# Performance work log

Measured on AMD Instinct MI355X. Metric: run time of the kernel, lower is better.

The kernel has to match this reference:

```python
import jax, jax.numpy as jnp
import numpy as np

B, T, D, R = 8, 2048, 2048, 4


def setup_inputs() -> dict:
    key = jax.random.key(0)
    ks = jax.random.split(key, 9)
    u = jax.random.normal(ks[0], (B, T, D), dtype=jnp.float32)
    # a chosen so tanh(a) ~ 0.995: keeps cumprod over T=2048 away from underflow
    a = 3.0 + 0.2 * jax.random.uniform(ks[1], (D,), dtype=jnp.float32)
    b = 0.02 * jax.random.normal(ks[2], (D,), dtype=jnp.float32)
    c = 0.02 * jax.random.normal(ks[3], (D,), dtype=jnp.float32)
    d = 0.02 * jax.random.normal(ks[4], (D,), dtype=jnp.float32)
    gate_w = jax.random.normal(ks[5], (D, D), dtype=jnp.float32) / np.float32(np.sqrt(D))
    gate_b = jnp.zeros((D,), dtype=jnp.float32)
    d_lr_u = 0.02 * jax.random.normal(ks[6], (D, R), dtype=jnp.float32)
    d_lr_v = 0.02 * jax.random.normal(ks[7], (R, D), dtype=jnp.float32)
    return {"u": u, "a": a, "b": b, "c": c, "d": d,
            "gate_w": gate_w, "gate_b": gate_b,
            "d_lr_u": d_lr_u, "d_lr_v": d_lr_v}


def reference(u, a, b, c, d, gate_w, gate_b, d_lr_u, d_lr_v):
    # u: [B,T,D]
    Bs, Ts, Ds = u.shape
    rank = d_lr_u.shape[1]
    # gated input (torch Linear: x @ W.T + bias)
    g = jax.nn.sigmoid(jnp.einsum('btd,ed->bte', u, gate_w) + gate_b)
    u_g = u * g
    aa = jnp.tanh(a)                                   # [D], in (-1,1)
    # low-rank correction to feedthrough d
    u_mean = jnp.mean(u_g, axis=1, keepdims=True)      # [B,1,D]
    d_lr = (u_mean @ d_lr_u) @ d_lr_v / max(1.0, float(rank))
    d_eff = d + d_lr                                   # [B,1,D]
    # diagonal SSM via cumprod/cumsum (G[t] = aa^(t+1)); per-channel, T-independent of B
    G = jnp.cumprod(jnp.broadcast_to(aa, (Ts, Ds)), axis=0)  # [T,D]
    bu = b * u_g                                       # [B,T,D]
    G_safe = G.at[0].set(jnp.maximum(G[0], 1e-6))
    z = bu / G_safe                                    # [B,T,D]
    s = G * jnp.cumsum(z, axis=1)                      # [B,T,D]
    y = c * s + d_eff * u_g
    return y
```

## Files before the change

kernel.cpp:

```cpp
#include <hip/hip_runtime.h>
#include <hip/hip_bf16.h>
#include <math.h>

#define Bq 8
#define Tq 2048
#define Dq 2048
#define Rq 4
#define Mq (Bq*Tq)
#define NC 16
#define CL (Tq/NC)

typedef __attribute__((ext_vector_type(8))) short bf16x8;
typedef __attribute__((ext_vector_type(4))) float f32x4;
typedef __attribute__((ext_vector_type(4))) unsigned short us4;

__device__ __forceinline__ unsigned short f2bf(float x) {
    unsigned int u = __float_as_uint(x);
    unsigned int r = (u + 0x7fffu + ((u >> 16) & 1u)) >> 16;
    return (unsigned short)r;
}
__device__ __forceinline__ float bf2f(unsigned short h) {
    return __uint_as_float((unsigned)h << 16);
}

template<int UGBF>
__device__ __forceinline__ f32x4 ld4(const void* p, long long off) {
    if constexpr (UGBF) {
        us4 v = *(const us4*)((const unsigned short*)p + off);
        f32x4 r;
        r.x = bf2f(v.x); r.y = bf2f(v.y); r.z = bf2f(v.z); r.w = bf2f(v.w);
        return r;
    } else {
        return *(const f32x4*)((const float*)p + off);
    }
}

__global__ __launch_bounds__(256) void k0_convert(
    const float* __restrict__ u, const float* __restrict__ gw,
    const float* __restrict__ a,
    unsigned short* __restrict__ ubf, unsigned short* __restrict__ wbf,
    float* __restrict__ aat, float* __restrict__ aaLt)
{
    const long long uN4 = (long long)Mq * Dq / 4;
    const long long wN4 = (long long)Dq * Dq / 4;
    long long gid = (long long)blockIdx.x * blockDim.x + threadIdx.x;
    if (gid < Dq) {
        float aa = tanhf(a[gid]);
        aat[gid] = aa;
        aaLt[gid] = exp2f((float)CL * log2f(aa));
    }
    long long stride = (long long)gridDim.x * blockDim.x;
    for (long long i = gid; i < uN4 + wN4; i += stride) {
        const float4* src; unsigned short* dst; long long j;
        if (i < uN4) { src = (const float4*)u;  dst = ubf; j = i; }
        else         { src = (const float4*)gw; dst = wbf; j = i - uN4; }
        float4 v = src[j];
        us4 p;
        p.x = f2bf(v.x); p.y = f2bf(v.y); p.z = f2bf(v.z); p.w = f2bf(v.w);
        *(us4*)(dst + j * 4) = p;
    }
}


#define PH_BAR __builtin_amdgcn_s_barrier()
#define PRIO1  __builtin_amdgcn_s_setprio(1)
#define PRIO0  __builtin_amdgcn_s_setprio(0)

#define LDA(BASE, qb) do { _Pragma("unroll") for (int f_ = 0; f_ < 4; ++f_) \
    { _Pragma("unroll") for (int ks_ = 0; ks_ < 2; ++ks_) \
        aF[ks_][f_] = *(const bf16x8*)&lds[(BASE) + ks_ * 4096 + ((qb) + f_) * 512]; } } while (0)

#define LDB(BASE, fnb) do { _Pragma("unroll") for (int f_ = 0; f_ < 2; ++f_) \
    { _Pragma("unroll") for (int ks_ = 0; ks_ < 2; ++ks_) \
        bF[ks_][(fnb) + f_] = *(const bf16x8*)&lds[(BASE) + ks_ * 4096 + ((fnb) + f_) * 512]; } } while (0)

#define MMA(fmb, fnb) do { _Pragma("unroll") for (int fm_ = 0; fm_ < 4; ++fm_) \
    _Pragma("unroll") for (int fn_ = 0; fn_ < 2; ++fn_) \
    _Pragma("unroll") for (int ks_ = 0; ks_ < 2; ++ks_) \
        acc[(fmb) + fm_][(fnb) + fn_] = __builtin_amdgcn_mfma_f32_16x16x32_bf16( \
            aF[ks_][fm_], bF[ks_][(fnb) + fn_], acc[(fmb) + fm_][(fnb) + fn_], 0, 0, 0); } while (0)

#define STAGE(G0, G1, OPB, DB, KOFF) do { _Pragma("unroll") for (int h_ = 0; h_ < 2; ++h_) { \
    const unsigned short* gp_ = h_ ? (G1) : (G0); \
    _Pragma("unroll") for (int ks_ = 0; ks_ < 2; ++ks_) { \
        __builtin_amdgcn_global_load_lds( \
            (const __attribute__((address_space(1))) void*)(gp_ + (KOFF) + ks_ * 32), \
            (__attribute__((address_space(3))) void*)&lds[(DB) * 32768 + (OPB) + h_ * 8192 + ks_ * 4096 + wave * 512], \
            16, 0, 0); } } } while (0)

template<int UGBF>
__global__ __launch_bounds__(512, 2) void k1_gemm(
    const unsigned short* __restrict__ Abf,
    const unsigned short* __restrict__ Bbf,
    const float* __restrict__ gate_b,
    void* __restrict__ ug_)
{
    __shared__ unsigned short lds[65536];
    const int tid  = threadIdx.x;
    const int wave = tid >> 6, lane = tid & 63;
    const int wr = wave >> 2, wc = wave & 3;

    const int bid = blockIdx.x;
    const int swz = (bid & 7) * 64 + (bid >> 3);
    const int tm = (swz >> 3) * 256;
    const int tn = (swz & 7) * 256;

    const int rr = lane & 15, kq = lane >> 4, kb = kq * 8;
    const int lp = lane ^ ((lane >> 4) & 2);
    const int srow = lp >> 2;
    const int scol = (lp & 3) * 8;

    const int swA0 = (wr * 8192 + rr * 32 + kb) ^ ((rr & 8) << 1);
    const int swA1 = swA0 + 32768;
    const int swB0 = (16384 + (wc >> 1) * 8192 + (wc & 1) * 2048 + rr * 32 + kb) ^ ((rr & 8) << 1);
    const int swB1 = swB0 + 32768;

    const unsigned short* gA0 = Abf + (long long)(tm + wave * 16 + srow) * Dq + scol;
    const unsigned short* gA1 = gA0 + 128 * Dq;
    const unsigned short* gB0 = Bbf + (long long)(tn + wave * 16 + srow) * Dq + scol;
    const unsigned short* gB1 = gB0 + 128 * Dq;

    f32x4 acc[8][4] = {};
    bf16x8 aF[2][4], bF[2][4];

    STAGE(gB0, gB1, 16384, 0, 0);
    STAGE(gA0, gA1, 0,     0, 0);
    STAGE(gB0, gB1, 16384, 1, 64);
    STAGE(gA0, gA1, 0,     1, 64);
    asm volatile("s_waitcnt vmcnt(8)" ::: "memory");
    PH_BAR;

    const int NIT = Dq / 128;
    for (int it = 0; it < NIT; ++it) {
        const bool pre = (it < NIT - 1);

        LDA(swA0, 0); LDB(swB0, 0);
        PH_BAR; PRIO1; MMA(0, 0); PRIO0; PH_BAR;
        LDB(swB0, 2);
        PH_BAR; PRIO1; MMA(0, 2); PRIO0; PH_BAR;
        LDA(swA0, 4);
        if (pre) STAGE(gB0, gB1, 16384, 0, 128);
        PH_BAR; PRIO1; MMA(4, 0); PRIO0; PH_BAR;
        if (pre) STAGE(gA0, gA1, 0, 0, 128);
        PH_BAR;
        if (pre) asm volatile("s_waitcnt vmcnt(8)" ::: "memory");
        else     asm volatile("s_waitcnt vmcnt(0)" ::: "memory");
        PRIO1; MMA(4, 2); PRIO0; PH_BAR;

        LDA(swA1, 0); LDB(swB1, 0);
        PH_BAR; PRIO1; MMA(0, 0); PRIO0; PH_BAR;
        LDB(swB1, 2);
        PH_BAR; PRIO1; MMA(0, 2); PRIO0; PH_BAR;
        LDA(swA1, 4);
        if (pre) STAGE(gB0, gB1, 16384, 1, 192);
        PH_BAR; PRIO1; MMA(4, 0); PRIO0; PH_BAR;
        if (pre) STAGE(gA0, gA1, 0, 1, 192);
        PH_BAR;
        if (pre) asm volatile("s_waitcnt vmcnt(8)" ::: "memory");
        else     asm volatile("s_waitcnt vmcnt(0)" ::: "memory");
        PRIO1; MMA(4, 2); PRIO0; PH_BAR;

        gA0 += 128; gA1 += 128; gB0 += 128; gB1 += 128;
    }

#pragma unroll
    for (int fm = 0; fm < 8; ++fm) {
#pragma unroll
        for (int fn = 0; fn < 4; ++fn) {
            const int col = tn + wc * 64 + fn * 16 + rr;
            const float gb = gate_b[col];
#pragma unroll
            for (int j = 0; j < 4; ++j) {
                const int row = tm + wr * 128 + fm * 16 + kq * 4 + j;
                const long long idx = (long long)row * Dq + col;
                const float logit = acc[fm][fn][j] + gb;
                const float s = 1.0f / (1.0f + __expf(-logit));
                const float uv = bf2f(Abf[idx]);
                if constexpr (UGBF) ((unsigned short*)ug_)[idx] = f2bf(uv * s);
                else                ((float*)ug_)[idx] = uv * s;
            }
        }
    }
}

template<int UGBF>
__global__ __launch_bounds__(128) void k2_scanA(
    const void* __restrict__ ug, const float* __restrict__ aat,
    const float* __restrict__ bvec,
    float* __restrict__ psum, float* __restrict__ carry)
{
    const int d0 = blockIdx.x * 512 + threadIdx.x * 4;
    const int ck = blockIdx.y, bb = blockIdx.z;
    f32x4 aa = *(const f32x4*)&aat[d0];
    f32x4 bv = *(const f32x4*)&bvec[d0];
    f32x4 s = {0.f, 0.f, 0.f, 0.f}, sum = {0.f, 0.f, 0.f, 0.f};
    const long long base = ((long long)bb * Tq + (long long)ck * CL) * Dq + d0;
    for (int t = 0; t < CL; ++t) {
        f32x4 x = ld4<UGBF>(ug, base + (long long)t * Dq);
        sum += x;
        s = aa * s + bv * x;
    }
    long long ci = ((long long)bb * NC + ck) * Dq + d0;
    *(f32x4*)&psum[ci]  = sum;
    *(f32x4*)&carry[ci] = s;
}

__global__ __launch_bounds__(256) void k3_deff(
    const float* __restrict__ psum, const float* __restrict__ dvec,
    const float* __restrict__ dlru, const float* __restrict__ dlrv,
    float* __restrict__ deff)
{
    const int bb = blockIdx.x, tid = threadIdx.x;
    __shared__ float red[4][256];
    __shared__ float proj[4];
    float pr[4] = {0.f, 0.f, 0.f, 0.f};
    for (int i = 0; i < Dq / 256; ++i) {
        int dd = tid + i * 256;
        float m = 0.f;
        for (int k = 0; k < NC; ++k) m += psum[((long long)bb * NC + k) * Dq + dd];
        m *= (1.0f / (float)Tq);
#pragma unroll
        for (int r = 0; r < 4; ++r) pr[r] += m * dlru[dd * Rq + r];
    }
#pragma unroll
    for (int r = 0; r < 4; ++r) red[r][tid] = pr[r];
    __syncthreads();
    for (int off = 128; off > 0; off >>= 1) {
        if (tid < off)
#pragma unroll
            for (int r = 0; r < 4; ++r) red[r][tid] += red[r][tid + off];
        __syncthreads();
    }
    if (tid < 4) proj[tid] = red[tid][0] * 0.25f;
    __syncthreads();
    float p0 = proj[0], p1 = proj[1], p2 = proj[2], p3 = proj[3];
    for (int i = 0; i < Dq / 256; ++i) {
        int e = tid + i * 256;
        float v = dvec[e] + p0 * dlrv[0 * Dq + e] + p1 * dlrv[1 * Dq + e]
                          + p2 * dlrv[2 * Dq + e] + p3 * dlrv[3 * Dq + e];
        deff[(long long)bb * Dq + e] = v;
    }
}

template<int UGBF>
__global__ __launch_bounds__(128) void k4_scanC(
    const void* __restrict__ ug, float* __restrict__ yout,
    const float* __restrict__ aat, const float* __restrict__ aaLt,
    const float* __restrict__ bvec, const float* __restrict__ cvec,
    const float* __restrict__ deff, const float* __restrict__ carry)
{
    const int d0 = blockIdx.x * 512 + threadIdx.x * 4;
    const int ck = blockIdx.y, bb = blockIdx.z;
    f32x4 aa  = *(const f32x4*)&aat[d0];
    f32x4 aaL = *(const f32x4*)&aaLt[d0];
    f32x4 bv  = *(const f32x4*)&bvec[d0];
    f32x4 cv  = *(const f32x4*)&cvec[d0];
    f32x4 de  = *(const f32x4*)&deff[(long long)bb * Dq + d0];
    f32x4 s = {0.f, 0.f, 0.f, 0.f};
    for (int j = 0; j < ck; ++j) {
        f32x4 cj = *(const f32x4*)&carry[((long long)bb * NC + j) * Dq + d0];
        s = aaL * s + cj;
    }
    const long long base = ((long long)bb * Tq + (long long)ck * CL) * Dq + d0;
    for (int t = 0; t < CL; ++t) {
        f32x4 x = ld4<UGBF>(ug, base + (long long)t * Dq);
        s = aa * s + bv * x;
        f32x4 y = cv * s + de * x;
        *(f32x4*)&yout[base + (long long)t * Dq] = y;
    }
}

extern "C" void kernel_launch(void* const* d_in, const int* in_sizes, int n_in,
                              void* d_out, int out_size, void* d_ws, size_t ws_size,
                              hipStream_t stream)
{
    const float* u    = (const float*)d_in[0];
    const float* a    = (const float*)d_in[1];
    const float* b    = (const float*)d_in[2];
    const float* c    = (const float*)d_in[3];
    const float* d    = (const float*)d_in[4];
    const float* gw   = (const float*)d_in[5];
    const float* gb   = (const float*)d_in[6];
    const float* dlru = (const float*)d_in[7];
    const float* dlrv = (const float*)d_in[8];
    float* out = (float*)d_out;

    char* ws = (char*)d_ws;
    const size_t sz_ubf = (size_t)Mq * Dq * 2;
    const size_t sz_wbf = (size_t)Dq * Dq * 2;
    const size_t sz_ug  = (size_t)Mq * Dq * 2;
    const size_t sz_ps  = (size_t)Bq * NC * Dq * 4;

    unsigned short* ubf = (unsigned short*)ws;
    unsigned short* wbf = (unsigned short*)(ws + sz_ubf);

    const size_t need_bf16 = sz_ubf + sz_wbf + sz_ug + 2 * sz_ps
                           + (size_t)Bq * Dq * 4 + 2 * (size_t)Dq * 4;
    const bool ugbf_mode = (ws_size >= need_bf16);

    char* rest = ws + sz_ubf + sz_wbf;
    unsigned short* ugbf = (unsigned short*)rest;
    char* tail = ugbf_mode ? (rest + sz_ug) : rest;
    float* psum  = (float*)tail;
    float* carry = psum  + (size_t)Bq * NC * Dq;
    float* deff  = carry + (size_t)Bq * NC * Dq;
    float* aat   = deff  + (size_t)Bq * Dq;
    float* aaLt  = aat   + Dq;

    k0_convert<<<2048, 256, 0, stream>>>(u, gw, a, ubf, wbf, aat, aaLt);

    dim3 g2(Dq / 512, NC, Bq);
    if (ugbf_mode) {
        k1_gemm<1><<<512, 512, 0, stream>>>(ubf, wbf, gb, ugbf);
        k2_scanA<1><<<g2, 128, 0, stream>>>(ugbf, aat, b, psum, carry);
        k3_deff<<<Bq, 256, 0, stream>>>(psum, d, dlru, dlrv, deff);
        k4_scanC<1><<<g2, 128, 0, stream>>>(ugbf, out, aat, aaLt, b, c, deff, carry);
    } else {
        k1_gemm<0><<<512, 512, 0, stream>>>(ubf, wbf, gb, out);
        k2_scanA<0><<<g2, 128, 0, stream>>>(out, aat, b, psum, carry);
        k3_deff<<<Bq, 256, 0, stream>>>(psum, d, dlru, dlrv, deff);
        k4_scanC<0><<<g2, 128, 0, stream>>>(out, out, aat, aaLt, b, c, deff, carry);
    }
}
```

Measured before the change: 229.4 us.

## Fuse chunk scan partials into GEMM epilogue via LDS-staged sigmoid tile

The separate scanA kernel is removed. The GEMM epilogue now stages sigmoid gates as bf16 in LDS and re-reads them in a coalesced row layout. It then computes u*g, writes it out with vectorized stores, and accumulates per-chunk sums and decayed carries, using precomputed powers of aa and a strided-row decomposition reduced through LDS. This avoids a full extra read of the u_g tensor and one kernel launch, at the cost of a longer epilogue, extra LDS traffic and storing the gate in bf16, which reduces precision in fp32 mode.

```diff
diff --git a/kernel.cpp b/kernel.cpp
--- a/kernel.cpp
+++ b/kernel.cpp
@@ -13,6 +13,7 @@
 typedef __attribute__((ext_vector_type(8))) short bf16x8;
 typedef __attribute__((ext_vector_type(4))) float f32x4;
 typedef __attribute__((ext_vector_type(4))) unsigned short us4;
+typedef __attribute__((ext_vector_type(8))) unsigned short us8;
 
 __device__ __forceinline__ unsigned short f2bf(float x) {
     unsigned int u = __float_as_uint(x);
@@ -39,7 +40,8 @@
     const float* __restrict__ u, const float* __restrict__ gw,
     const float* __restrict__ a,
     unsigned short* __restrict__ ubf, unsigned short* __restrict__ wbf,
-    float* __restrict__ aat, float* __restrict__ aaLt)
+    float* __restrict__ aat, float* __restrict__ aaLt,
+    float* __restrict__ aapow)
 {
     const long long uN4 = (long long)Mq * Dq / 4;
     const long long wN4 = (long long)Dq * Dq / 4;
@@ -48,6 +50,8 @@
         float aa = tanhf(a[gid]);
         aat[gid] = aa;
         aaLt[gid] = exp2f((float)CL * log2f(aa));
+        float p = 1.0f;
+        for (int k = 0; k <= 16; ++k) { aapow[k * Dq + gid] = p; p *= aa; }
     }
     long long stride = (long long)gridDim.x * blockDim.x;
     for (long long i = gid; i < uN4 + wN4; i += stride) {
@@ -93,6 +97,10 @@
     const unsigned short* __restrict__ Abf,
     const unsigned short* __restrict__ Bbf,
     const float* __restrict__ gate_b,
+    const float* __restrict__ bvec,
+    const float* __restrict__ aapow,
+    float* __restrict__ psum,
+    float* __restrict__ carry,
     void* __restrict__ ug_)
 {
     __shared__ unsigned short lds[65536];
@@ -164,45 +172,96 @@
     }
 
 #pragma unroll
-    for (int fm = 0; fm < 8; ++fm) {
-#pragma unroll
-        for (int fn = 0; fn < 4; ++fn) {
-            const int col = tn + wc * 64 + fn * 16 + rr;
-            const float gb = gate_b[col];
+    for (int fn = 0; fn < 4; ++fn) {
+        const int col = wc * 64 + fn * 16 + rr;
+        const float gb = gate_b[tn + col];
+#pragma unroll
+        for (int fm = 0; fm < 8; ++fm) {
 #pragma unroll
             for (int j = 0; j < 4; ++j) {
-                const int row = tm + wr * 128 + fm * 16 + kq * 4 + j;
-                const long long idx = (long long)row * Dq + col;
+                const int row = wr * 128 + fm * 16 + kq * 4 + j;
                 const float logit = acc[fm][fn][j] + gb;
-                const float s = 1.0f / (1.0f + __expf(-logit));
-                const float uv = bf2f(Abf[idx]);
-                if constexpr (UGBF) ((unsigned short*)ug_)[idx] = f2bf(uv * s);
-                else                ((float*)ug_)[idx] = uv * s;
+                const float sg = 1.0f / (1.0f + __expf(-logit));
+                lds[row * 256 + (col ^ (kq << 4))] = f2bf(sg);
             }
         }
     }
-}
-
-template<int UGBF>
-__global__ __launch_bounds__(128) void k2_scanA(
-    const void* __restrict__ ug, const float* __restrict__ aat,
-    const float* __restrict__ bvec,
-    float* __restrict__ psum, float* __restrict__ carry)
-{
-    const int d0 = blockIdx.x * 512 + threadIdx.x * 4;
-    const int ck = blockIdx.y, bb = blockIdx.z;
-    f32x4 aa = *(const f32x4*)&aat[d0];
-    f32x4 bv = *(const f32x4*)&bvec[d0];
-    f32x4 s = {0.f, 0.f, 0.f, 0.f}, sum = {0.f, 0.f, 0.f, 0.f};
-    const long long base = ((long long)bb * Tq + (long long)ck * CL) * Dq + d0;
-    for (int t = 0; t < CL; ++t) {
-        f32x4 x = ld4<UGBF>(ug, base + (long long)t * Dq);
-        sum += x;
-        s = aa * s + bv * x;
-    }
-    long long ci = ((long long)bb * NC + ck) * Dq + d0;
-    *(f32x4*)&psum[ci]  = sum;
-    *(f32x4*)&carry[ci] = s;
+    __syncthreads();
+
+    const int lr2  = lane >> 5;
+    const int cb32 = lane & 31;
+    const int c0   = cb32 * 8;
+    const int baseT = wave * 2 + lr2;
+    const int cX = ((baseT >> 2) & 3) << 4;
+
+    float bw[8], a16[8], w15[8];
+    {
+        const float* bp   = bvec + tn + c0;
+        const float* a16p = aapow + 16 * Dq + tn + c0;
+        const float* w15p = aapow + (15 - baseT) * Dq + tn + c0;
+#pragma unroll
+        for (int k = 0; k < 8; ++k) { bw[k] = bp[k]; a16[k] = a16p[k]; w15[k] = w15p[k]; }
+    }
+
+    float ps[2][8] = {}, cr[2][8] = {};
+#pragma unroll
+    for (int i = 0; i < 16; ++i) {
+        const int r = baseT + i * 16;
+        const int ck = i >> 3;
+        const long long gidx = (long long)(tm + r) * Dq + tn + c0;
+        const bf16x8 u8 = *(const bf16x8*)&Abf[gidx];
+        const bf16x8 s8 = *(const bf16x8*)&lds[r * 256 + (c0 ^ cX)];
+        float ug[8];
+#pragma unroll
+        for (int k = 0; k < 8; ++k) {
+            ug[k] = bf2f((unsigned short)u8[k]) * bf2f((unsigned short)s8[k]);
+            ps[ck][k] += ug[k];
+            cr[ck][k] = a16[k] * cr[ck][k] + bw[k] * ug[k];
+        }
+        if constexpr (UGBF) {
+            us8 o;
+#pragma unroll
+            for (int k = 0; k < 8; ++k) o[k] = f2bf(ug[k]);
+            *(us8*)&((unsigned short*)ug_)[gidx] = o;
+        } else {
+            f32x4 o0, o1;
+            o0.x = ug[0]; o0.y = ug[1]; o0.z = ug[2]; o0.w = ug[3];
+            o1.x = ug[4]; o1.y = ug[5]; o1.z = ug[6]; o1.w = ug[7];
+            *(f32x4*)&((float*)ug_)[gidx]     = o0;
+            *(f32x4*)&((float*)ug_)[gidx + 4] = o1;
+        }
+    }
+    __syncthreads();
+
+    float* redf = (float*)lds;
+    const int slot = (baseT + cb32) & 15;
+#pragma unroll
+    for (int ck = 0; ck < 2; ++ck)
+#pragma unroll
+        for (int k = 0; k < 8; ++k) {
+            const int col = c0 + k;
+            redf[((ck * 2 + 0) * 256 + col) * 16 + slot] = ps[ck][k];
+            redf[((ck * 2 + 1) * 256 + col) * 16 + slot] = cr[ck][k] * w15[k];
+        }
+    __syncthreads();
+
+    const int bb  = tm >> 11;
+    const int ckb = (tm & 2047) >> 7;
+#pragma unroll
+    for (int ii = 0; ii < 2; ++ii) {
+        const int item = tid + ii * 512;
+        const int p = item >> 8, col = item & 255;
+        const int ck = p >> 1, isC = p & 1;
+        const int rot = (item & 3) * 4;
+        float s = 0.f;
+#pragma unroll
+        for (int q = 0; q < 4; ++q) {
+            const f32x4 v = *(const f32x4*)&redf[item * 16 + ((rot + q * 4) & 15)];
+            s += v.x + v.y + v.z + v.w;
+        }
+        const long long gi = (long long)(bb * NC + ckb + ck) * Dq + tn + col;
+        if (isC) carry[gi] = s; else psum[gi] = s;
+    }
 }
 
 __global__ __launch_bounds__(256) void k3_deff(
@@ -294,8 +353,9 @@
     unsigned short* ubf = (unsigned short*)ws;
     unsigned short* wbf = (unsigned short*)(ws + sz_ubf);
 
-    const size_t need_bf16 = sz_ubf + sz_wbf + sz_ug + 2 * sz_ps
-                           + (size_t)Bq * Dq * 4 + 2 * (size_t)Dq * 4;
+    const size_t tail_sz = 2 * sz_ps + (size_t)Bq * Dq * 4
+                         + 2 * (size_t)Dq * 4 + (size_t)17 * Dq * 4;
+    const size_t need_bf16 = sz_ubf + sz_wbf + sz_ug + tail_sz;
     const bool ugbf_mode = (ws_size >= need_bf16);
 
     char* rest = ws + sz_ubf + sz_wbf;
@@ -306,18 +366,17 @@
     float* deff  = carry + (size_t)Bq * NC * Dq;
     float* aat   = deff  + (size_t)Bq * Dq;
     float* aaLt  = aat   + Dq;
-
-    k0_convert<<<2048, 256, 0, stream>>>(u, gw, a, ubf, wbf, aat, aaLt);
+    float* aapow = aaLt  + Dq;
+
+    k0_convert<<<2048, 256, 0, stream>>>(u, gw, a, ubf, wbf, aat, aaLt, aapow);
 
     dim3 g2(Dq / 512, NC, Bq);
     if (ugbf_mode) {
-        k1_gemm<1><<<512, 512, 0, stream>>>(ubf, wbf, gb, ugbf);
-        k2_scanA<1><<<g2, 128, 0, stream>>>(ugbf, aat, b, psum, carry);
+        k1_gemm<1><<<512, 512, 0, stream>>>(ubf, wbf, gb, b, aapow, psum, carry, ugbf);
         k3_deff<<<Bq, 256, 0, stream>>>(psum, d, dlru, dlrv, deff);
         k4_scanC<1><<<g2, 128, 0, stream>>>(ugbf, out, aat, aaLt, b, c, deff, carry);
     } else {
-        k1_gemm<0><<<512, 512, 0, stream>>>(ubf, wbf, gb, out);
-        k2_scanA<0><<<g2, 128, 0, stream>>>(out, aat, b, psum, carry);
+        k1_gemm<0><<<512, 512, 0, stream>>>(ubf, wbf, gb, b, aapow, psum, carry, out);
         k3_deff<<<Bq, 256, 0, stream>>>(psum, d, dlru, dlrv, deff);
         k4_scanC<0><<<g2, 128, 0, stream>>>(out, out, aat, aaLt, b, c, deff, carry);
     }
```

New measurement: 240.3 us. 1.05x slower.
